# Performance work log

Measured on AMD Instinct MI355X. Metric: run time of the kernel, lower is better.

Reference implementation:

```python
import jax, jax.numpy as jnp
import numpy as np

B, S, D = 8, 2048, 256
EXP = 4
NEG = -1e9
EPS = 1e-5


def layer_norm(x, w, b):
    mu = jnp.mean(x, axis=-1, keepdims=True)
    var = jnp.var(x, axis=-1, keepdims=True)
    return (x - mu) * jax.lax.rsqrt(var + EPS) * w + b


def setup_inputs() -> dict:
    key = jax.random.key(0)
    ks = jax.random.split(key, 8)
    x = jax.random.normal(ks[0], (B, S, D), dtype=jnp.float32)
    r_mat = jax.random.normal(ks[1], (B, S, S), dtype=jnp.float32)
    attn_mask = jax.random.randint(ks[2], (S, S), 0, 2).astype(jnp.float32)
    pad_mask = jax.random.randint(ks[3], (B, 1, S), 0, 2).astype(jnp.float32)
    w1 = jax.random.normal(ks[4], (D, EXP * D), dtype=jnp.float32) / np.sqrt(D)
    b1 = jnp.zeros((EXP * D,), dtype=jnp.float32)
    w2 = jax.random.normal(ks[5], (EXP * D, D), dtype=jnp.float32) / np.sqrt(EXP * D)
    b2 = jnp.zeros((D,), dtype=jnp.float32)
    ln1_w = jnp.ones((D,), dtype=jnp.float32)
    ln1_b = jnp.zeros((D,), dtype=jnp.float32)
    ln2_w = jnp.ones((D,), dtype=jnp.float32)
    ln2_b = jnp.zeros((D,), dtype=jnp.float32)
    return {"x": x, "r_mat": r_mat, "attn_mask": attn_mask, "pad_mask": pad_mask,
            "ln1_w": ln1_w, "ln1_b": ln1_b, "ln2_w": ln2_w, "ln2_b": ln2_b,
            "w1": w1, "b1": b1, "w2": w2, "b2": b2}


def reference(x, r_mat, attn_mask, pad_mask, ln1_w, ln1_b, ln2_w, ln2_b, w1, b1, w2, b2):
    # sublayer 0: pre-LN + InrAwaSA + residual
    h = layer_norm(x, ln1_w, ln1_b)                       # [B,S,D]
    scale = jnp.sqrt(jnp.float32(D))
    scores = jnp.einsum("bqd,bkd->bqk", h, h) / scale      # [B,S,S]
    # mask r_mat by pad_mask [B,1,S] and attn_mask [1,S,S], then softmax
    rm = jnp.where(pad_mask == 0.0, NEG, r_mat)
    rm = jnp.where(attn_mask[None] == 0.0, NEG, rm)
    scores = scores + jax.nn.softmax(rm, axis=-1)
    # NOTE: the torch source calls scores.masked_fill(...) non-in-place and
    # discards the result, so scores are NOT re-masked here (faithful no-op).
    prob = jax.nn.softmax(scores, axis=-1)
    x = x + jnp.einsum("bqk,bkd->bqd", prob, h)
    # sublayer 1: pre-LN + FFN + residual (dropout is identity in eval)
    h2 = layer_norm(x, ln2_w, ln2_b)
    ffn = jax.nn.relu(h2 @ w1 + b1) @ w2 + b2
    return x + ffn
```

## Files before the change

### kernel.cpp

```cpp
#include <hip/hip_runtime.h>
#include <stdint.h>

#define NB 8
#define SS 2048
#define DD 256
#define NEGV -1e9f
#define LDSW 136

typedef __attribute__((ext_vector_type(8))) __bf16 bf16x8;
typedef __attribute__((ext_vector_type(4))) float f32x4;

union U16 { uint4 u; bf16x8 b; unsigned short us[8]; };

__device__ __forceinline__ unsigned short tobf(float v) {
  union { float f; uint32_t u; } c; c.f = v;
  uint32_t r = (c.u + 0x7fffu + ((c.u >> 16) & 1u)) >> 16;
  return (unsigned short)r;
}
__device__ __forceinline__ float frombf(unsigned short v) {
  union { uint32_t u; float f; } c; c.u = ((uint32_t)v) << 16;
  return c.f;
}

__device__ __forceinline__ void glds16(const unsigned short* g, unsigned short* l) {
  __builtin_amdgcn_global_load_lds(
      (const __attribute__((address_space(1))) uint32_t*)g,
      (__attribute__((address_space(3))) uint32_t*)l, 16, 0, 0);
}

__device__ __forceinline__ void stage_tile(const unsigned short* src, int ld,
                                           unsigned short* lbuf, int w, int lane) {
  int rl = lane >> 2;
  int cs = (lane & 3) * 8;
  glds16(src + (size_t)(w * 32 + rl) * ld + cs, lbuf + w * 1024);
  glds16(src + (size_t)(w * 32 + 16 + rl) * ld + cs, lbuf + w * 1024 + 512);
}

template <int NSTEPS>
__device__ __forceinline__ void gemm128_tile(
    const unsigned short* __restrict__ A, int lda,
    const unsigned short* __restrict__ Bt, int ldb,
    unsigned short* smem, f32x4 (&acc)[4][4]) {
  unsigned short* lA = smem;
  unsigned short* lB = smem + 8192;
  const int w = threadIdx.x >> 6, lane = threadIdx.x & 63;
  const int lr = lane & 15, lg = lane >> 4;
  const int wm = w >> 1, wn = w & 1;
#pragma unroll
  for (int i = 0; i < 4; ++i)
#pragma unroll
    for (int j = 0; j < 4; ++j) acc[i][j] = (f32x4){0.f, 0.f, 0.f, 0.f};
  stage_tile(A, lda, lA, w, lane);
  stage_tile(Bt, ldb, lB, w, lane);
  __syncthreads();
  for (int s = 0; s < NSTEPS; ++s) {
    const unsigned short* cA = lA + (s & 1) * 4096;
    const unsigned short* cB = lB + (s & 1) * 4096;
    if (s + 1 < NSTEPS) {
      stage_tile(A + (s + 1) * 32, lda, lA + ((s + 1) & 1) * 4096, w, lane);
      stage_tile(Bt + (s + 1) * 32, ldb, lB + ((s + 1) & 1) * 4096, w, lane);
    }
    bf16x8 am[4], bn[4];
#pragma unroll
    for (int i = 0; i < 4; ++i) {
      U16 u; u.u = *(const uint4*)(cA + (wm * 64 + i * 16 + lr) * 32 + lg * 8);
      am[i] = u.b;
      U16 v; v.u = *(const uint4*)(cB + (wn * 64 + i * 16 + lr) * 32 + lg * 8);
      bn[i] = v.b;
    }
#pragma unroll
    for (int i = 0; i < 4; ++i)
#pragma unroll
      for (int j = 0; j < 4; ++j)
        acc[i][j] = __builtin_amdgcn_mfma_f32_16x16x32_bf16(am[i], bn[j], acc[i][j], 0, 0, 0);
    __syncthreads();
  }
}

template <int NSTEPS>
__device__ __forceinline__ void gemm256_acc(
    const unsigned short* __restrict__ A, int lda,
    const unsigned short* __restrict__ Bt, int ldb,
    unsigned short* smem, f32x4 (&acc)[4][4]) {
  unsigned short* lA = smem;
  unsigned short* lB = smem + 8192;
  const int tid = threadIdx.x;
  const int w = tid >> 6, lane = tid & 63;
  const int lr = lane & 15, lg = lane >> 4;
  const int wm = w >> 2, wn = w & 3;
  const int rl = lane >> 2, cs = (lane & 3) * 8;
#pragma unroll
  for (int i = 0; i < 4; ++i)
#pragma unroll
    for (int j = 0; j < 4; ++j) acc[i][j] = (f32x4){0.f, 0.f, 0.f, 0.f};
  glds16(A + (size_t)(w * 16 + rl) * lda + cs, lA + w * 512);
  glds16(Bt + (size_t)(w * 32 + rl) * ldb + cs, lB + w * 1024);
  glds16(Bt + (size_t)(w * 32 + 16 + rl) * ldb + cs, lB + w * 1024 + 512);
  __syncthreads();
  for (int s = 0; s < NSTEPS; ++s) {
    const unsigned short* cA = lA + (s & 1) * 4096;
    const unsigned short* cB = lB + (s & 1) * 8192;
    if (s + 1 < NSTEPS) {
      const unsigned short* An = A + (s + 1) * 32;
      const unsigned short* Bn = Bt + (s + 1) * 32;
      glds16(An + (size_t)(w * 16 + rl) * lda + cs, lA + ((s + 1) & 1) * 4096 + w * 512);
      glds16(Bn + (size_t)(w * 32 + rl) * ldb + cs, lB + ((s + 1) & 1) * 8192 + w * 1024);
      glds16(Bn + (size_t)(w * 32 + 16 + rl) * ldb + cs,
             lB + ((s + 1) & 1) * 8192 + w * 1024 + 512);
    }
    bf16x8 am[4], bn[4];
#pragma unroll
    for (int i = 0; i < 4; ++i) {
      U16 u; u.u = *(const uint4*)(cA + (wm * 64 + i * 16 + lr) * 32 + lg * 8);
      am[i] = u.b;
      U16 v; v.u = *(const uint4*)(cB + (wn * 64 + i * 16 + lr) * 32 + lg * 8);
      bn[i] = v.b;
    }
#pragma unroll
    for (int i = 0; i < 4; ++i)
#pragma unroll
      for (int j = 0; j < 4; ++j)
        acc[i][j] = __builtin_amdgcn_mfma_f32_16x16x32_bf16(am[i], bn[j], acc[i][j], 0, 0, 0);
    __syncthreads();
  }
}

__global__ void ln_kernel(const float* __restrict__ in, const float* __restrict__ w,
                          const float* __restrict__ bparm, unsigned short* __restrict__ outb) {
  int row = blockIdx.x * 4 + (threadIdx.x >> 6);
  int lane = threadIdx.x & 63;
  const float* xr = in + (size_t)row * DD;
  float4 v = *(const float4*)(xr + lane * 4);
  float s = v.x + v.y + v.z + v.w;
  float s2 = v.x * v.x + v.y * v.y + v.z * v.z + v.w * v.w;
#pragma unroll
  for (int m = 1; m < 64; m <<= 1) { s += __shfl_xor(s, m); s2 += __shfl_xor(s2, m); }
  float mu = s * (1.f / DD);
  float var = s2 * (1.f / DD) - mu * mu;
  float rs = rsqrtf(var + 1e-5f);
  float4 wv = *(const float4*)(w + lane * 4);
  float4 bv = *(const float4*)(bparm + lane * 4);
  ushort4 o;
  o.x = tobf((v.x - mu) * rs * wv.x + bv.x);
  o.y = tobf((v.y - mu) * rs * wv.y + bv.y);
  o.z = tobf((v.z - mu) * rs * wv.z + bv.z);
  o.w = tobf((v.w - mu) * rs * wv.w + bv.w);
  *(ushort4*)(outb + (size_t)row * DD + lane * 4) = o;
}

__global__ void transpose_kernel(const unsigned short* __restrict__ in,
                                 unsigned short* __restrict__ out) {
  __shared__ unsigned short tile[64][72];
  int bid = blockIdx.x;
  int b = bid >> 7;
  int rest = bid & 127;
  int st = rest >> 2, dt = rest & 3;
  int s0 = st * 64, d0 = dt * 64;
  int t = threadIdx.x;
  int r = t >> 2, cs = (t & 3) * 16;
  const unsigned short* src = in + ((size_t)b * SS + s0 + r) * DD + d0 + cs;
  *(uint4*)&tile[r][cs] = *(const uint4*)src;
  *(uint4*)&tile[r][cs + 8] = *(const uint4*)(src + 8);
  __syncthreads();
  union { unsigned short us[16]; uint4 u[2]; } tmp;
  int dr = t >> 2, sseg = (t & 3) * 16;
#pragma unroll
  for (int j = 0; j < 16; ++j) tmp.us[j] = tile[sseg + j][dr];
  unsigned short* dst = out + ((size_t)b * DD + d0 + dr) * SS + s0 + sseg;
  *(uint4*)dst = tmp.u[0];
  *(uint4*)(dst + 8) = tmp.u[1];
}

__global__ __launch_bounds__(256) void qk_kernel(
    const unsigned short* __restrict__ hb,
    unsigned short* __restrict__ S) {
  __shared__ unsigned short smem[17408];
  int bid = blockIdx.x;
  int b = bid & 7;
  int t = bid >> 3;
  int mb = 0, rem = t;
  while (rem >= 16 - mb) { rem -= 16 - mb; ++mb; }
  int nb = mb + rem;
  const unsigned short* A = hb + (size_t)(b * SS + mb * 128) * DD;
  const unsigned short* Bt = hb + (size_t)(b * SS + nb * 128) * DD;
  f32x4 acc[4][4];
  gemm128_tile<8>(A, DD, Bt, DD, smem, acc);
  int tid = threadIdx.x;
  int w = tid >> 6, lane = tid & 63;
  int lr = lane & 15, lg = lane >> 4;
  int wm = w >> 1, wn = w & 1;
  unsigned short* Sb = S + (size_t)b * SS * SS;
#pragma unroll
  for (int i = 0; i < 4; ++i)
#pragma unroll
    for (int j = 0; j < 4; ++j)
#pragma unroll
      for (int r = 0; r < 4; ++r) {
        int m = mb * 128 + wm * 64 + i * 16 + lg * 4 + r;
        int n = nb * 128 + wn * 64 + j * 16 + lr;
        Sb[(size_t)m * SS + n] = tobf(acc[i][j][r] * 0.0625f);
      }
  if (mb != nb) {
#pragma unroll
    for (int i = 0; i < 4; ++i)
#pragma unroll
      for (int j = 0; j < 4; ++j) {
        int col = wn * 64 + j * 16 + lr;
#pragma unroll
        for (int r = 0; r < 4; ++r) {
          int row = wm * 64 + i * 16 + lg * 4 + r;
          smem[col * LDSW + row] = tobf(acc[i][j][r] * 0.0625f);
        }
      }
    __syncthreads();
    int row2 = tid >> 1, half = (tid & 1) * 64;
    const unsigned short* s = smem + row2 * LDSW + half;
    unsigned short* d = Sb + (size_t)(nb * 128 + row2) * SS + mb * 128 + half;
    uint4 vv[8];
#pragma unroll
    for (int k = 0; k < 8; ++k) vv[k] = *(const uint4*)(s + k * 8);
#pragma unroll
    for (int k = 0; k < 8; ++k) *(uint4*)(d + k * 8) = vv[k];
  }
}

__global__ __launch_bounds__(256) void smfuse_kernel(
    const float* __restrict__ r_mat,
    const float* __restrict__ attn,
    const float* __restrict__ pad,
    unsigned short* __restrict__ S) {
  int row = blockIdx.x * 4 + (threadIdx.x >> 6);
  int lane = threadIdx.x & 63;
  int b = row >> 11, q = row & 2047;
  const float* rrow = r_mat + (size_t)row * SS;
  const float* arow = attn + (size_t)q * SS;
  const float* prow = pad + (size_t)b * SS;
  unsigned short* srow = S + (size_t)row * SS;

  float rm[32];
  float mx = -__builtin_inff();
#pragma unroll
  for (int i = 0; i < 8; ++i) {
    int c = i * 256 + lane * 4;
    float4 rv = *(const float4*)(rrow + c);
    float4 av = *(const float4*)(arow + c);
    float4 pv = *(const float4*)(prow + c);
    float v0 = (pv.x == 0.f || av.x == 0.f) ? NEGV : rv.x;
    float v1 = (pv.y == 0.f || av.y == 0.f) ? NEGV : rv.y;
    float v2 = (pv.z == 0.f || av.z == 0.f) ? NEGV : rv.z;
    float v3 = (pv.w == 0.f || av.w == 0.f) ? NEGV : rv.w;
    rm[i * 4 + 0] = v0; rm[i * 4 + 1] = v1; rm[i * 4 + 2] = v2; rm[i * 4 + 3] = v3;
    mx = fmaxf(mx, fmaxf(fmaxf(v0, v1), fmaxf(v2, v3)));
  }
#pragma unroll
  for (int m = 1; m < 64; m <<= 1) mx = fmaxf(mx, __shfl_xor(mx, m));
  float sum = 0.f;
#pragma unroll
  for (int j = 0; j < 32; ++j) { rm[j] = __expf(rm[j] - mx); sum += rm[j]; }
#pragma unroll
  for (int m = 1; m < 64; m <<= 1) sum += __shfl_xor(sum, m);
  float inv = 1.f / sum;

  float sc[32];
  float mx2 = -__builtin_inff();
#pragma unroll
  for (int i = 0; i < 8; ++i) {
    int c = i * 256 + lane * 4;
    ushort4 sv = *(const ushort4*)(srow + c);
    float s0 = frombf(sv.x) + rm[i * 4 + 0] * inv;
    float s1 = frombf(sv.y) + rm[i * 4 + 1] * inv;
    float s2 = frombf(sv.z) + rm[i * 4 + 2] * inv;
    float s3 = frombf(sv.w) + rm[i * 4 + 3] * inv;
    sc[i * 4 + 0] = s0; sc[i * 4 + 1] = s1; sc[i * 4 + 2] = s2; sc[i * 4 + 3] = s3;
    mx2 = fmaxf(mx2, fmaxf(fmaxf(s0, s1), fmaxf(s2, s3)));
  }
#pragma unroll
  for (int m = 1; m < 64; m <<= 1) mx2 = fmaxf(mx2, __shfl_xor(mx2, m));
  float sum2 = 0.f;
#pragma unroll
  for (int j = 0; j < 32; ++j) { sc[j] = __expf(sc[j] - mx2); sum2 += sc[j]; }
#pragma unroll
  for (int m = 1; m < 64; m <<= 1) sum2 += __shfl_xor(sum2, m);
  float inv2 = 1.f / sum2;
#pragma unroll
  for (int i = 0; i < 8; ++i) {
    int c = i * 256 + lane * 4;
    ushort4 o;
    o.x = tobf(sc[i * 4 + 0] * inv2);
    o.y = tobf(sc[i * 4 + 1] * inv2);
    o.z = tobf(sc[i * 4 + 2] * inv2);
    o.w = tobf(sc[i * 4 + 3] * inv2);
    *(ushort4*)(srow + c) = o;
  }
}

__global__ __launch_bounds__(512) void pv_kernel(
    const unsigned short* __restrict__ P,
    const unsigned short* __restrict__ hbT,
    unsigned short* __restrict__ pvp) {
  __shared__ unsigned short smem[24576];
  int bid = blockIdx.x;
  int b = bid & 7;
  int rest = bid >> 3;
  int ks = rest & 3, mb = rest >> 2;
  const unsigned short* A = P + (size_t)(b * SS + mb * 128) * SS + ks * 512;
  const unsigned short* Bt = hbT + (size_t)(b * DD) * SS + ks * 512;
  f32x4 acc[4][4];
  gemm256_acc<16>(A, SS, Bt, SS, smem, acc);
  int w = threadIdx.x >> 6, lane = threadIdx.x & 63;
  int lr = lane & 15, lg = lane >> 4;
  int wm = w >> 2, wn = w & 3;
  unsigned short* O = pvp + ((size_t)(ks << 14) + (b << 11) + mb * 128) * DD;
#pragma unroll
  for (int i = 0; i < 4; ++i)
#pragma unroll
    for (int j = 0; j < 4; ++j)
#pragma unroll
      for (int r = 0; r < 4; ++r) {
        int m = wm * 64 + i * 16 + lg * 4 + r;
        int n = wn * 64 + j * 16 + lr;
        O[(size_t)m * DD + n] = tobf(acc[i][j][r]);
      }
}

__global__ __launch_bounds__(256) void pvreduce_kernel(
    const unsigned short* __restrict__ pvp,
    const float* __restrict__ x,
    const float* __restrict__ ln2w,
    const float* __restrict__ ln2b,
    float* __restrict__ out,
    unsigned short* __restrict__ h2b) {
  int r = blockIdx.x * 4 + (threadIdx.x >> 6);
  int lane = threadIdx.x & 63;
  int c = lane * 4;
  float o[4] = {0.f, 0.f, 0.f, 0.f};
#pragma unroll
  for (int ks = 0; ks < 4; ++ks) {
    ushort4 pk = *(const ushort4*)(pvp + ((size_t)(ks << 14) + r) * DD + c);
    o[0] += frombf(pk.x); o[1] += frombf(pk.y);
    o[2] += frombf(pk.z); o[3] += frombf(pk.w);
  }
  float4 xv = *(const float4*)(x + (size_t)r * DD + c);
  float val[4] = {o[0] + xv.x, o[1] + xv.y, o[2] + xv.z, o[3] + xv.w};
  float4 ov = {val[0], val[1], val[2], val[3]};
  *(float4*)(out + (size_t)r * DD + c) = ov;
  float s = val[0] + val[1] + val[2] + val[3];
  float s2 = val[0] * val[0] + val[1] * val[1] + val[2] * val[2] + val[3] * val[3];
#pragma unroll
  for (int m = 1; m < 64; m <<= 1) { s += __shfl_xor(s, m); s2 += __shfl_xor(s2, m); }
  float mu = s * (1.f / DD);
  float var = s2 * (1.f / DD) - mu * mu;
  float rsv = rsqrtf(var + 1e-5f);
  float4 wv = *(const float4*)(ln2w + c);
  float4 bv = *(const float4*)(ln2b + c);
  ushort4 h;
  h.x = tobf((val[0] - mu) * rsv * wv.x + bv.x);
  h.y = tobf((val[1] - mu) * rsv * wv.y + bv.y);
  h.z = tobf((val[2] - mu) * rsv * wv.z + bv.z);
  h.w = tobf((val[3] - mu) * rsv * wv.w + bv.w);
  *(ushort4*)(h2b + (size_t)r * DD + c) = h;
}

__global__ void wconv_kernel(const float* __restrict__ w1, unsigned short* __restrict__ w1bT,
                             const float* __restrict__ w2, unsigned short* __restrict__ w2bT) {
  __shared__ unsigned short tile[64][72];
  int bid = blockIdx.x;
  const float* src; unsigned short* dst; int K, N, t;
  if (bid < 64) { src = w1; dst = w1bT; K = 256; N = 1024; t = bid; }
  else          { src = w2; dst = w2bT; K = 1024; N = 256; t = bid - 64; }
  int nt = N >> 6;
  int kt = t / nt, ntb = t % nt;
  int k0 = kt * 64, n0 = ntb * 64;
  int tt = threadIdx.x;
  int r = tt >> 2, c4 = (tt & 3) * 16;
  const float* s = src + (size_t)(k0 + r) * N + n0 + c4;
#pragma unroll
  for (int j = 0; j < 16; ++j) tile[r][c4 + j] = tobf(s[j]);
  __syncthreads();
  union { unsigned short us[16]; uint4 u[2]; } tmp;
  int nr = tt >> 2, ks = (tt & 3) * 16;
#pragma unroll
  for (int j = 0; j < 16; ++j) tmp.us[j] = tile[ks + j][nr];
  unsigned short* d = dst + (size_t)(n0 + nr) * K + k0 + ks;
  *(uint4*)d = tmp.u[0];
  *(uint4*)(d + 8) = tmp.u[1];
}

__global__ __launch_bounds__(512) void ffn1_kernel(
    const unsigned short* __restrict__ A0,
    const unsigned short* __restrict__ Bt0,
    const float* __restrict__ bias,
    unsigned short* __restrict__ Out) {
  __shared__ unsigned short smem[24576];
  int bid = blockIdx.x;
  int nb = bid & 3, mb = bid >> 2;
  const unsigned short* A = A0 + (size_t)(mb * 128) * 256;
  const unsigned short* Bt = Bt0 + (size_t)(nb * 256) * 256;
  f32x4 acc[4][4];
  gemm256_acc<8>(A, 256, Bt, 256, smem, acc);
  int w = threadIdx.x >> 6, lane = threadIdx.x & 63;
  int lr = lane & 15, lg = lane >> 4;
  int wm = w >> 2, wn = w & 3;
#pragma unroll
  for (int i = 0; i < 4; ++i)
#pragma unroll
    for (int j = 0; j < 4; ++j)
#pragma unroll
      for (int r = 0; r < 4; ++r) {
        int m = mb * 128 + wm * 64 + i * 16 + lg * 4 + r;
        int n = nb * 256 + wn * 64 + j * 16 + lr;
        float v = fmaxf(acc[i][j][r] + bias[n], 0.f);
        Out[(size_t)m * 1024 + n] = tobf(v);
      }
}

__global__ __launch_bounds__(512) void ffn2_kernel(
    const unsigned short* __restrict__ A0,
    const unsigned short* __restrict__ Bt0,
    unsigned short* __restrict__ f2p) {
  __shared__ unsigned short smem[24576];
  int bid = blockIdx.x;
  int ks = bid & 3, mb = bid >> 2;
  const unsigned short* A = A0 + (size_t)(mb * 128) * 1024 + ks * 256;
  const unsigned short* Bt = Bt0 + ks * 256;
  f32x4 acc[4][4];
  gemm256_acc<8>(A, 1024, Bt, 1024, smem, acc);
  int w = threadIdx.x >> 6, lane = threadIdx.x & 63;
  int lr = lane & 15, lg = lane >> 4;
  int wm = w >> 2, wn = w & 3;
  unsigned short* O = f2p + ((size_t)(ks << 14) + mb * 128) * DD;
#pragma unroll
  for (int i = 0; i < 4; ++i)
#pragma unroll
    for (int j = 0; j < 4; ++j)
#pragma unroll
      for (int r = 0; r < 4; ++r) {
        int m = wm * 64 + i * 16 + lg * 4 + r;
        int n = wn * 64 + j * 16 + lr;
        O[(size_t)m * DD + n] = tobf(acc[i][j][r]);
      }
}

__global__ __launch_bounds__(256) void f2reduce_kernel(
    const unsigned short* __restrict__ f2p,
    const float* __restrict__ bias,
    float* __restrict__ out) {
  int r = blockIdx.x * 4 + (threadIdx.x >> 6);
  int lane = threadIdx.x & 63;
  int c = lane * 4;
  float o[4] = {0.f, 0.f, 0.f, 0.f};
#pragma unroll
  for (int ks = 0; ks < 4; ++ks) {
    ushort4 pk = *(const ushort4*)(f2p + ((size_t)(ks << 14) + r) * DD + c);
    o[0] += frombf(pk.x); o[1] += frombf(pk.y);
    o[2] += frombf(pk.z); o[3] += frombf(pk.w);
  }
  float4 bv = *(const float4*)(bias + c);
  float* orow = out + (size_t)r * DD + c;
  float4 cur = *(const float4*)orow;
  float4 res = {cur.x + o[0] + bv.x, cur.y + o[1] + bv.y,
                cur.z + o[2] + bv.z, cur.w + o[3] + bv.w};
  *(float4*)orow = res;
}

extern "C" void kernel_launch(void* const* d_in, const int* in_sizes, int n_in,
                              void* d_out, int out_size, void* d_ws, size_t ws_size,
                              hipStream_t stream) {
  const float* x     = (const float*)d_in[0];
  const float* r_mat = (const float*)d_in[1];
  const float* attn  = (const float*)d_in[2];
  const float* pad   = (const float*)d_in[3];
  const float* ln1w  = (const float*)d_in[4];
  const float* ln1b  = (const float*)d_in[5];
  const float* ln2w  = (const float*)d_in[6];
  const float* ln2b  = (const float*)d_in[7];
  const float* w1    = (const float*)d_in[8];
  const float* b1    = (const float*)d_in[9];
  const float* w2    = (const float*)d_in[10];
  const float* b2    = (const float*)d_in[11];
  float* out = (float*)d_out;

  uint8_t* ws = (uint8_t*)d_ws;
  unsigned short* hb   = (unsigned short*)(ws + 0);
  unsigned short* hbT  = (unsigned short*)(ws + 8388608);
  unsigned short* h2b  = (unsigned short*)(ws + 16777216);
  unsigned short* w1bT = (unsigned short*)(ws + 25165824);
  unsigned short* w2bT = (unsigned short*)(ws + 25690112);
  unsigned short* S    = (unsigned short*)(ws + 33554432);
  unsigned short* pvp  = (unsigned short*)(ws + 100663296);
  unsigned short* t    = S;
  unsigned short* f2p  = pvp;

  hipLaunchKernelGGL(ln_kernel, dim3(4096), dim3(256), 0, stream, x, ln1w, ln1b, hb);
  hipLaunchKernelGGL(transpose_kernel, dim3(1024), dim3(256), 0, stream, hb, hbT);
  hipLaunchKernelGGL(qk_kernel, dim3(1088), dim3(256), 0, stream, hb, S);
  hipLaunchKernelGGL(smfuse_kernel, dim3(4096), dim3(256), 0, stream, r_mat, attn, pad, S);
  hipLaunchKernelGGL(pv_kernel, dim3(512), dim3(512), 0, stream, S, hbT, pvp);
  hipLaunchKernelGGL(pvreduce_kernel, dim3(4096), dim3(256), 0, stream,
                     pvp, x, ln2w, ln2b, out, h2b);
  hipLaunchKernelGGL(wconv_kernel, dim3(128), dim3(256), 0, stream, w1, w1bT, w2, w2bT);
  hipLaunchKernelGGL(ffn1_kernel, dim3(512), dim3(512), 0, stream, h2b, w1bT, b1, t);
  hipLaunchKernelGGL(ffn2_kernel, dim3(512), dim3(512), 0, stream, t, w2bT, f2p);
  hipLaunchKernelGGL(f2reduce_kernel, dim3(4096), dim3(256), 0, stream, f2p, b2, out);
}
```

Baseline: 186.0 us.

## Merge independent stages into shared launches and split mask-softmax from QK

LayerNorm and the weight conversion now share one launch. The transpose, the QK^T GEMM and the masked r_mat softmax run as block ranges of a single kernel, so the memory-bound r_mat softmax can overlap with the compute-bound GEMM. The r_mat softmax result is written to a new bf16 workspace buffer and read back by a second softmax kernel. This cuts launch count and tail idle time, but it adds an extra write and read of a B*S*S bf16 tensor and rounds the first softmax to bf16.

```diff
diff --git a/kernel.cpp b/kernel.cpp
--- a/kernel.cpp
+++ b/kernel.cpp
@@ -125,152 +125,196 @@
   }
 }
 
-__global__ void ln_kernel(const float* __restrict__ in, const float* __restrict__ w,
-                          const float* __restrict__ bparm, unsigned short* __restrict__ outb) {
-  int row = blockIdx.x * 4 + (threadIdx.x >> 6);
-  int lane = threadIdx.x & 63;
-  const float* xr = in + (size_t)row * DD;
-  float4 v = *(const float4*)(xr + lane * 4);
-  float s = v.x + v.y + v.z + v.w;
-  float s2 = v.x * v.x + v.y * v.y + v.z * v.z + v.w * v.w;
-#pragma unroll
-  for (int m = 1; m < 64; m <<= 1) { s += __shfl_xor(s, m); s2 += __shfl_xor(s2, m); }
-  float mu = s * (1.f / DD);
-  float var = s2 * (1.f / DD) - mu * mu;
-  float rs = rsqrtf(var + 1e-5f);
-  float4 wv = *(const float4*)(w + lane * 4);
-  float4 bv = *(const float4*)(bparm + lane * 4);
-  ushort4 o;
-  o.x = tobf((v.x - mu) * rs * wv.x + bv.x);
-  o.y = tobf((v.y - mu) * rs * wv.y + bv.y);
-  o.z = tobf((v.z - mu) * rs * wv.z + bv.z);
-  o.w = tobf((v.w - mu) * rs * wv.w + bv.w);
-  *(ushort4*)(outb + (size_t)row * DD + lane * 4) = o;
-}
-
-__global__ void transpose_kernel(const unsigned short* __restrict__ in,
-                                 unsigned short* __restrict__ out) {
+__global__ __launch_bounds__(256) void lnw_kernel(
+    const float* __restrict__ in, const float* __restrict__ w,
+    const float* __restrict__ bparm, unsigned short* __restrict__ outb,
+    const float* __restrict__ w1, unsigned short* __restrict__ w1bT,
+    const float* __restrict__ w2, unsigned short* __restrict__ w2bT) {
   __shared__ unsigned short tile[64][72];
   int bid = blockIdx.x;
-  int b = bid >> 7;
-  int rest = bid & 127;
-  int st = rest >> 2, dt = rest & 3;
-  int s0 = st * 64, d0 = dt * 64;
-  int t = threadIdx.x;
-  int r = t >> 2, cs = (t & 3) * 16;
-  const unsigned short* src = in + ((size_t)b * SS + s0 + r) * DD + d0 + cs;
-  *(uint4*)&tile[r][cs] = *(const uint4*)src;
-  *(uint4*)&tile[r][cs + 8] = *(const uint4*)(src + 8);
-  __syncthreads();
-  union { unsigned short us[16]; uint4 u[2]; } tmp;
-  int dr = t >> 2, sseg = (t & 3) * 16;
-#pragma unroll
-  for (int j = 0; j < 16; ++j) tmp.us[j] = tile[sseg + j][dr];
-  unsigned short* dst = out + ((size_t)b * DD + d0 + dr) * SS + s0 + sseg;
-  *(uint4*)dst = tmp.u[0];
-  *(uint4*)(dst + 8) = tmp.u[1];
-}
-
-__global__ __launch_bounds__(256) void qk_kernel(
+  if (bid < 4096) {
+    int row = bid * 4 + (threadIdx.x >> 6);
+    int lane = threadIdx.x & 63;
+    const float* xr = in + (size_t)row * DD;
+    float4 v = *(const float4*)(xr + lane * 4);
+    float s = v.x + v.y + v.z + v.w;
+    float s2 = v.x * v.x + v.y * v.y + v.z * v.z + v.w * v.w;
+#pragma unroll
+    for (int m = 1; m < 64; m <<= 1) { s += __shfl_xor(s, m); s2 += __shfl_xor(s2, m); }
+    float mu = s * (1.f / DD);
+    float var = s2 * (1.f / DD) - mu * mu;
+    float rs = rsqrtf(var + 1e-5f);
+    float4 wv = *(const float4*)(w + lane * 4);
+    float4 bv = *(const float4*)(bparm + lane * 4);
+    ushort4 o;
+    o.x = tobf((v.x - mu) * rs * wv.x + bv.x);
+    o.y = tobf((v.y - mu) * rs * wv.y + bv.y);
+    o.z = tobf((v.z - mu) * rs * wv.z + bv.z);
+    o.w = tobf((v.w - mu) * rs * wv.w + bv.w);
+    *(ushort4*)(outb + (size_t)row * DD + lane * 4) = o;
+  } else {
+    int t = bid - 4096;
+    const float* src; unsigned short* dst; int K, N;
+    if (t < 64) { src = w1; dst = w1bT; K = 256; N = 1024; }
+    else        { src = w2; dst = w2bT; K = 1024; N = 256; t -= 64; }
+    int nt = N >> 6;
+    int kt = t / nt, ntb = t % nt;
+    int k0 = kt * 64, n0 = ntb * 64;
+    int tt = threadIdx.x;
+    int r = tt >> 2, c4 = (tt & 3) * 16;
+    const float* s = src + (size_t)(k0 + r) * N + n0 + c4;
+#pragma unroll
+    for (int j = 0; j < 16; ++j) tile[r][c4 + j] = tobf(s[j]);
+    __syncthreads();
+    union { unsigned short us[16]; uint4 u[2]; } tmp;
+    int nr = tt >> 2, ks = (tt & 3) * 16;
+#pragma unroll
+    for (int j = 0; j < 16; ++j) tmp.us[j] = tile[ks + j][nr];
+    unsigned short* d = dst + (size_t)(n0 + nr) * K + k0 + ks;
+    *(uint4*)d = tmp.u[0];
+    *(uint4*)(d + 8) = tmp.u[1];
+  }
+}
+
+__global__ __launch_bounds__(256) void fused_kernel(
     const unsigned short* __restrict__ hb,
-    unsigned short* __restrict__ S) {
-  __shared__ unsigned short smem[17408];
-  int bid = blockIdx.x;
-  int b = bid & 7;
-  int t = bid >> 3;
-  int mb = 0, rem = t;
-  while (rem >= 16 - mb) { rem -= 16 - mb; ++mb; }
-  int nb = mb + rem;
-  const unsigned short* A = hb + (size_t)(b * SS + mb * 128) * DD;
-  const unsigned short* Bt = hb + (size_t)(b * SS + nb * 128) * DD;
-  f32x4 acc[4][4];
-  gemm128_tile<8>(A, DD, Bt, DD, smem, acc);
-  int tid = threadIdx.x;
-  int w = tid >> 6, lane = tid & 63;
-  int lr = lane & 15, lg = lane >> 4;
-  int wm = w >> 1, wn = w & 1;
-  unsigned short* Sb = S + (size_t)b * SS * SS;
-#pragma unroll
-  for (int i = 0; i < 4; ++i)
-#pragma unroll
-    for (int j = 0; j < 4; ++j)
-#pragma unroll
-      for (int r = 0; r < 4; ++r) {
-        int m = mb * 128 + wm * 64 + i * 16 + lg * 4 + r;
-        int n = nb * 128 + wn * 64 + j * 16 + lr;
-        Sb[(size_t)m * SS + n] = tobf(acc[i][j][r] * 0.0625f);
-      }
-  if (mb != nb) {
-#pragma unroll
-    for (int i = 0; i < 4; ++i)
-#pragma unroll
-      for (int j = 0; j < 4; ++j) {
-        int col = wn * 64 + j * 16 + lr;
-#pragma unroll
-        for (int r = 0; r < 4; ++r) {
-          int row = wm * 64 + i * 16 + lg * 4 + r;
-          smem[col * LDSW + row] = tobf(acc[i][j][r] * 0.0625f);
-        }
-      }
-    __syncthreads();
-    int row2 = tid >> 1, half = (tid & 1) * 64;
-    const unsigned short* s = smem + row2 * LDSW + half;
-    unsigned short* d = Sb + (size_t)(nb * 128 + row2) * SS + mb * 128 + half;
-    uint4 vv[8];
-#pragma unroll
-    for (int k = 0; k < 8; ++k) vv[k] = *(const uint4*)(s + k * 8);
-#pragma unroll
-    for (int k = 0; k < 8; ++k) *(uint4*)(d + k * 8) = vv[k];
-  }
-}
-
-__global__ __launch_bounds__(256) void smfuse_kernel(
+    unsigned short* __restrict__ hbT,
+    unsigned short* __restrict__ S,
     const float* __restrict__ r_mat,
     const float* __restrict__ attn,
     const float* __restrict__ pad,
+    unsigned short* __restrict__ rmsm) {
+  __shared__ unsigned short smem[17408];
+  int bid = blockIdx.x;
+  if (bid < 1024) {
+    unsigned short (*tile)[72] = (unsigned short (*)[72])smem;
+    int b = bid >> 7;
+    int rest = bid & 127;
+    int st = rest >> 2, dt = rest & 3;
+    int s0 = st * 64, d0 = dt * 64;
+    int t = threadIdx.x;
+    int r = t >> 2, cs = (t & 3) * 16;
+    const unsigned short* src = hb + ((size_t)b * SS + s0 + r) * DD + d0 + cs;
+    *(uint4*)&tile[r][cs] = *(const uint4*)src;
+    *(uint4*)&tile[r][cs + 8] = *(const uint4*)(src + 8);
+    __syncthreads();
+    union { unsigned short us[16]; uint4 u[2]; } tmp;
+    int dr = t >> 2, sseg = (t & 3) * 16;
+#pragma unroll
+    for (int j = 0; j < 16; ++j) tmp.us[j] = tile[sseg + j][dr];
+    unsigned short* dst = hbT + ((size_t)b * DD + d0 + dr) * SS + s0 + sseg;
+    *(uint4*)dst = tmp.u[0];
+    *(uint4*)(dst + 8) = tmp.u[1];
+  } else if (bid < 2112) {
+    int t = bid - 1024;
+    int b = t & 7;
+    int tri = t >> 3;
+    int mb = 0, rem = tri;
+    while (rem >= 16 - mb) { rem -= 16 - mb; ++mb; }
+    int nb = mb + rem;
+    const unsigned short* A = hb + (size_t)(b * SS + mb * 128) * DD;
+    const unsigned short* Bt = hb + (size_t)(b * SS + nb * 128) * DD;
+    f32x4 acc[4][4];
+    gemm128_tile<8>(A, DD, Bt, DD, smem, acc);
+    int tid = threadIdx.x;
+    int w = tid >> 6, lane = tid & 63;
+    int lr = lane & 15, lg = lane >> 4;
+    int wm = w >> 1, wn = w & 1;
+    unsigned short* Sb = S + (size_t)b * SS * SS;
+#pragma unroll
+    for (int i = 0; i < 4; ++i)
+#pragma unroll
+      for (int j = 0; j < 4; ++j)
+#pragma unroll
+        for (int r = 0; r < 4; ++r) {
+          int m = mb * 128 + wm * 64 + i * 16 + lg * 4 + r;
+          int n = nb * 128 + wn * 64 + j * 16 + lr;
+          Sb[(size_t)m * SS + n] = tobf(acc[i][j][r] * 0.0625f);
+        }
+    if (mb != nb) {
+#pragma unroll
+      for (int i = 0; i < 4; ++i)
+#pragma unroll
+        for (int j = 0; j < 4; ++j) {
+          int col = wn * 64 + j * 16 + lr;
+#pragma unroll
+          for (int r = 0; r < 4; ++r) {
+            int row = wm * 64 + i * 16 + lg * 4 + r;
+            smem[col * LDSW + row] = tobf(acc[i][j][r] * 0.0625f);
+          }
+        }
+      __syncthreads();
+      int row2 = tid >> 1, half = (tid & 1) * 64;
+      const unsigned short* s = smem + row2 * LDSW + half;
+      unsigned short* d = Sb + (size_t)(nb * 128 + row2) * SS + mb * 128 + half;
+      uint4 vv[8];
+#pragma unroll
+      for (int k = 0; k < 8; ++k) vv[k] = *(const uint4*)(s + k * 8);
+#pragma unroll
+      for (int k = 0; k < 8; ++k) *(uint4*)(d + k * 8) = vv[k];
+    }
+  } else {
+    int row = (bid - 2112) * 4 + (threadIdx.x >> 6);
+    int lane = threadIdx.x & 63;
+    int b = row >> 11, q = row & 2047;
+    const float* rrow = r_mat + (size_t)row * SS;
+    const float* arow = attn + (size_t)q * SS;
+    const float* prow = pad + (size_t)b * SS;
+    float rm[32];
+    float mx = -__builtin_inff();
+#pragma unroll
+    for (int i = 0; i < 8; ++i) {
+      int c = i * 256 + lane * 4;
+      float4 rv = *(const float4*)(rrow + c);
+      float4 av = *(const float4*)(arow + c);
+      float4 pv = *(const float4*)(prow + c);
+      float v0 = (pv.x == 0.f || av.x == 0.f) ? NEGV : rv.x;
+      float v1 = (pv.y == 0.f || av.y == 0.f) ? NEGV : rv.y;
+      float v2 = (pv.z == 0.f || av.z == 0.f) ? NEGV : rv.z;
+      float v3 = (pv.w == 0.f || av.w == 0.f) ? NEGV : rv.w;
+      rm[i * 4 + 0] = v0; rm[i * 4 + 1] = v1; rm[i * 4 + 2] = v2; rm[i * 4 + 3] = v3;
+      mx = fmaxf(mx, fmaxf(fmaxf(v0, v1), fmaxf(v2, v3)));
+    }
+#pragma unroll
+    for (int m = 1; m < 64; m <<= 1) mx = fmaxf(mx, __shfl_xor(mx, m));
+    float sum = 0.f;
+#pragma unroll
+    for (int j = 0; j < 32; ++j) { rm[j] = __expf(rm[j] - mx); sum += rm[j]; }
+#pragma unroll
+    for (int m = 1; m < 64; m <<= 1) sum += __shfl_xor(sum, m);
+    float inv = 1.f / sum;
+    unsigned short* orow = rmsm + (size_t)row * SS;
+#pragma unroll
+    for (int i = 0; i < 8; ++i) {
+      int c = i * 256 + lane * 4;
+      ushort4 o;
+      o.x = tobf(rm[i * 4 + 0] * inv);
+      o.y = tobf(rm[i * 4 + 1] * inv);
+      o.z = tobf(rm[i * 4 + 2] * inv);
+      o.w = tobf(rm[i * 4 + 3] * inv);
+      *(ushort4*)(orow + c) = o;
+    }
+  }
+}
+
+__global__ __launch_bounds__(256) void smfuse2_kernel(
+    const unsigned short* __restrict__ rmsm,
     unsigned short* __restrict__ S) {
   int row = blockIdx.x * 4 + (threadIdx.x >> 6);
   int lane = threadIdx.x & 63;
-  int b = row >> 11, q = row & 2047;
-  const float* rrow = r_mat + (size_t)row * SS;
-  const float* arow = attn + (size_t)q * SS;
-  const float* prow = pad + (size_t)b * SS;
   unsigned short* srow = S + (size_t)row * SS;
-
-  float rm[32];
-  float mx = -__builtin_inff();
-#pragma unroll
-  for (int i = 0; i < 8; ++i) {
-    int c = i * 256 + lane * 4;
-    float4 rv = *(const float4*)(rrow + c);
-    float4 av = *(const float4*)(arow + c);
-    float4 pv = *(const float4*)(prow + c);
-    float v0 = (pv.x == 0.f || av.x == 0.f) ? NEGV : rv.x;
-    float v1 = (pv.y == 0.f || av.y == 0.f) ? NEGV : rv.y;
-    float v2 = (pv.z == 0.f || av.z == 0.f) ? NEGV : rv.z;
-    float v3 = (pv.w == 0.f || av.w == 0.f) ? NEGV : rv.w;
-    rm[i * 4 + 0] = v0; rm[i * 4 + 1] = v1; rm[i * 4 + 2] = v2; rm[i * 4 + 3] = v3;
-    mx = fmaxf(mx, fmaxf(fmaxf(v0, v1), fmaxf(v2, v3)));
-  }
-#pragma unroll
-  for (int m = 1; m < 64; m <<= 1) mx = fmaxf(mx, __shfl_xor(mx, m));
-  float sum = 0.f;
-#pragma unroll
-  for (int j = 0; j < 32; ++j) { rm[j] = __expf(rm[j] - mx); sum += rm[j]; }
-#pragma unroll
-  for (int m = 1; m < 64; m <<= 1) sum += __shfl_xor(sum, m);
-  float inv = 1.f / sum;
-
+  const unsigned short* mrow = rmsm + (size_t)row * SS;
   float sc[32];
   float mx2 = -__builtin_inff();
 #pragma unroll
   for (int i = 0; i < 8; ++i) {
     int c = i * 256 + lane * 4;
     ushort4 sv = *(const ushort4*)(srow + c);
-    float s0 = frombf(sv.x) + rm[i * 4 + 0] * inv;
-    float s1 = frombf(sv.y) + rm[i * 4 + 1] * inv;
-    float s2 = frombf(sv.z) + rm[i * 4 + 2] * inv;
-    float s3 = frombf(sv.w) + rm[i * 4 + 3] * inv;
+    ushort4 mv = *(const ushort4*)(mrow + c);
+    float s0 = frombf(sv.x) + frombf(mv.x);
+    float s1 = frombf(sv.y) + frombf(mv.y);
+    float s2 = frombf(sv.z) + frombf(mv.z);
+    float s3 = frombf(sv.w) + frombf(mv.w);
     sc[i * 4 + 0] = s0; sc[i * 4 + 1] = s1; sc[i * 4 + 2] = s2; sc[i * 4 + 3] = s3;
     mx2 = fmaxf(mx2, fmaxf(fmaxf(s0, s1), fmaxf(s2, s3)));
   }
@@ -361,31 +405,6 @@
   *(ushort4*)(h2b + (size_t)r * DD + c) = h;
 }
 
-__global__ void wconv_kernel(const float* __restrict__ w1, unsigned short* __restrict__ w1bT,
-                             const float* __restrict__ w2, unsigned short* __restrict__ w2bT) {
-  __shared__ unsigned short tile[64][72];
-  int bid = blockIdx.x;
-  const float* src; unsigned short* dst; int K, N, t;
-  if (bid < 64) { src = w1; dst = w1bT; K = 256; N = 1024; t = bid; }
-  else          { src = w2; dst = w2bT; K = 1024; N = 256; t = bid - 64; }
-  int nt = N >> 6;
-  int kt = t / nt, ntb = t % nt;
-  int k0 = kt * 64, n0 = ntb * 64;
-  int tt = threadIdx.x;
-  int r = tt >> 2, c4 = (tt & 3) * 16;
-  const float* s = src + (size_t)(k0 + r) * N + n0 + c4;
-#pragma unroll
-  for (int j = 0; j < 16; ++j) tile[r][c4 + j] = tobf(s[j]);
-  __syncthreads();
-  union { unsigned short us[16]; uint4 u[2]; } tmp;
-  int nr = tt >> 2, ks = (tt & 3) * 16;
-#pragma unroll
-  for (int j = 0; j < 16; ++j) tmp.us[j] = tile[ks + j][nr];
-  unsigned short* d = dst + (size_t)(n0 + nr) * K + k0 + ks;
-  *(uint4*)d = tmp.u[0];
-  *(uint4*)(d + 8) = tmp.u[1];
-}
-
 __global__ __launch_bounds__(512) void ffn1_kernel(
     const unsigned short* __restrict__ A0,
     const unsigned short* __restrict__ Bt0,
@@ -488,17 +507,18 @@
   unsigned short* w2bT = (unsigned short*)(ws + 25690112);
   unsigned short* S    = (unsigned short*)(ws + 33554432);
   unsigned short* pvp  = (unsigned short*)(ws + 100663296);
+  unsigned short* rmsm = (unsigned short*)(ws + 134217728);
   unsigned short* t    = S;
   unsigned short* f2p  = pvp;
 
-  hipLaunchKernelGGL(ln_kernel, dim3(4096), dim3(256), 0, stream, x, ln1w, ln1b, hb);
-  hipLaunchKernelGGL(transpose_kernel, dim3(1024), dim3(256), 0, stream, hb, hbT);
-  hipLaunchKernelGGL(qk_kernel, dim3(1088), dim3(256), 0, stream, hb, S);
-  hipLaunchKernelGGL(smfuse_kernel, dim3(4096), dim3(256), 0, stream, r_mat, attn, pad, S);
+  hipLaunchKernelGGL(lnw_kernel, dim3(4224), dim3(256), 0, stream,
+                     x, ln1w, ln1b, hb, w1, w1bT, w2, w2bT);
+  hipLaunchKernelGGL(fused_kernel, dim3(6208), dim3(256), 0, stream,
+                     hb, hbT, S, r_mat, attn, pad, rmsm);
+  hipLaunchKernelGGL(smfuse2_kernel, dim3(4096), dim3(256), 0, stream, rmsm, S);
   hipLaunchKernelGGL(pv_kernel, dim3(512), dim3(512), 0, stream, S, hbT, pvp);
   hipLaunchKernelGGL(pvreduce_kernel, dim3(4096), dim3(256), 0, stream,
                      pvp, x, ln2w, ln2b, out, h2b);
-  hipLaunchKernelGGL(wconv_kernel, dim3(128), dim3(256), 0, stream, w1, w1bT, w2, w2bT);
   hipLaunchKernelGGL(ffn1_kernel, dim3(512), dim3(512), 0, stream, h2b, w1bT, b1, t);
   hipLaunchKernelGGL(ffn2_kernel, dim3(512), dim3(512), 0, stream, t, w2bT, f2p);
   hipLaunchKernelGGL(f2reduce_kernel, dim3(4096), dim3(256), 0, stream, f2p, b2, out);
```

After: 203.1 us. +9.2%, slower.
